# Optimization experiments

Measured on AMD Instinct MI355X. Metric: run time of the kernel, lower is better.

Reference implementation:

```python
import jax, jax.numpy as jnp
import numpy as np

N, E, H, IN_DIM, EDGE_DIM = 100000, 1600000, 64, 1, 1
SLOPE = 0.01  # leaky_relu negative slope (torch default; GATConv negative_slope=0.01)


def _lrelu(v):
    return jax.nn.leaky_relu(v, SLOPE)


def _segment_softmax(a, idx, num_segments):
    a_max = jax.ops.segment_max(a, idx, num_segments=num_segments)
    e = jnp.exp(a - a_max[idx])
    denom = jax.ops.segment_sum(e, idx, num_segments=num_segments)
    return e / denom[idx]


def _gru_cell(x, h, w_ih, w_hh, b_ih, b_hh):
    # torch.nn.GRUCell: gates ordered r, z, n
    gi = x @ w_ih.T + b_ih
    gh = h @ w_hh.T + b_hh
    i_r, i_z, i_n = jnp.split(gi, 3, axis=-1)
    h_r, h_z, h_n = jnp.split(gh, 3, axis=-1)
    r = jax.nn.sigmoid(i_r + h_r)
    z = jax.nn.sigmoid(i_z + h_z)
    n = jnp.tanh(i_n + r * h_n)
    return (1.0 - z) * n + z * h


def setup_inputs():
    key = jax.random.key(0)
    ks = jax.random.split(key, 20)
    s = 0.1
    p = lambda i, shape: s * jax.random.normal(ks[i], shape, jnp.float32)
    z = lambda shape: jnp.zeros(shape, jnp.float32)
    return {
        "node_attr": jax.random.normal(ks[0], (N, IN_DIM), jnp.float32),
        "edge_attr": jax.random.normal(ks[1], (E, EDGE_DIM), jnp.float32),
        "edge_index": jax.random.randint(ks[2], (2, E), 0, N, jnp.int32),
        "w1": p(3, (H, IN_DIM)), "b1": z((H,)),
        "wg1": p(4, (H, H + EDGE_DIM)), "att_l": p(5, (H,)), "att_r": p(6, (H,)),
        "wg2": p(7, (H, H)), "bg": z((H,)),
        "gru1_wih": p(8, (3 * H, H)), "gru1_whh": p(9, (3 * H, H)),
        "gru1_bih": z((3 * H,)), "gru1_bhh": z((3 * H,)),
        "wm": p(10, (H, H)), "att_src": p(11, (H,)), "att_dst": p(12, (H,)),
        "bm": z((H,)),
        "gru2_wih": p(13, (3 * H, H)), "gru2_whh": p(14, (3 * H, H)),
        "gru2_bih": z((3 * H,)), "gru2_bhh": z((3 * H,)),
        "w2": p(15, (H, H)), "b2": z((H,)),
    }


def _forward(node_attr, edge_attr, edge_index, w1, b1, wg1, att_l, att_r, wg2, bg,
             gru1_wih, gru1_whh, gru1_bih, gru1_bhh,
             wm, att_src, att_dst, bm,
             gru2_wih, gru2_whh, gru2_bih, gru2_bhh, w2, b2):
    src, dst = edge_index[0], edge_index[1]
    # lin1 + in-place leaky_relu
    x = _lrelu(node_attr @ w1.T + b1)                                      # [N,H]
    # --- GATEConv: gather -> edge transform -> softmax over dst -> scatter-add ---
    h_e = _lrelu(jnp.concatenate([x[src], edge_attr], axis=-1) @ wg1.T)    # [E,H]
    a = _lrelu(h_e @ att_l + x[dst] @ att_r)                               # [E]
    alpha = _segment_softmax(a, dst, N)
    h = jax.ops.segment_sum((h_e @ wg2.T) * alpha[:, None], dst, num_segments=N) + bg
    x = jax.nn.relu(_gru_cell(jax.nn.elu(h), x, gru1_wih, gru1_whh, gru1_bih, gru1_bhh))
    # --- molecule readout: batch = zeros(N) -> single graph ---
    batch = jnp.zeros((x.shape[0],), jnp.int32)
    out = jax.nn.relu(jax.ops.segment_sum(x, batch, num_segments=1))       # [1,H]
    # GATConv over bipartite graph (every node -> its graph), shared lin, 1 head
    xs = x @ wm.T                                                          # [N,H]
    xd = out @ wm.T                                                        # [1,H]
    a2 = _lrelu(xs @ att_src + (xd @ att_dst)[batch])                      # [N]
    alpha2 = _segment_softmax(a2, batch, 1)
    h2 = jax.ops.segment_sum(xs * alpha2[:, None], batch, num_segments=1) + bm
    out = jax.nn.relu(_gru_cell(jax.nn.elu(h2), out, gru2_wih, gru2_whh, gru2_bih, gru2_bhh))
    return out @ w2.T + b2                                                 # [1,H]


def reference(node_attr, edge_attr, edge_index, w1, b1, wg1, att_l, att_r, wg2, bg,
              gru1_wih, gru1_whh, gru1_bih, gru1_bhh,
              wm, att_src, att_dst, bm,
              gru2_wih, gru2_whh, gru2_bih, gru2_bhh, w2, b2):
    return _forward(node_attr, edge_attr, edge_index, w1, b1, wg1, att_l, att_r, wg2, bg,
                    gru1_wih, gru1_whh, gru1_bih, gru1_bhh,
                    wm, att_src, att_dst, bm,
                    gru2_wih, gru2_whh, gru2_bih, gru2_bhh, w2, b2)
```

## Files before the change

kernel.cpp:

```cpp
#include <hip/hip_runtime.h>
#include <math.h>

typedef __attribute__((ext_vector_type(8))) short bf8;
typedef __attribute__((ext_vector_type(4))) float f32x4;

#define BSHIFT 8

__device__ __forceinline__ float lrelu(float v){ return fmaxf(v, 0.01f * v); }

__device__ __forceinline__ float wave_sum(float v){
#pragma unroll
  for (int s = 32; s > 0; s >>= 1) v += __shfl_xor(v, s);
  return v;
}
__device__ __forceinline__ float wave_max(float v){
#pragma unroll
  for (int s = 32; s > 0; s >>= 1) v = fmaxf(v, __shfl_xor(v, s));
  return v;
}

__device__ __forceinline__ float bcast(float v, int k){
  return __uint_as_float((unsigned)__builtin_amdgcn_readlane(__float_as_uint(v), k));
}

__device__ __forceinline__ unsigned fkey(float x){
  unsigned u = __float_as_uint(x);
  return (u & 0x80000000u) ? ~u : (u | 0x80000000u);
}
__device__ __forceinline__ float funkey(unsigned k){
  unsigned u = (k & 0x80000000u) ? (k & 0x7fffffffu) : ~k;
  return __uint_as_float(u);
}

__device__ __forceinline__ short f2bfs(float x){
  unsigned u = __float_as_uint(x);
  return (short)((u + 0x7fffu + ((u >> 16) & 1u)) >> 16);
}
__device__ __forceinline__ float bf2f(ushort v){
  return __uint_as_float((unsigned)v << 16);
}
__device__ __forceinline__ bf8 pack8(float4 a, float4 b){
  bf8 v;
  v[0]=f2bfs(a.x); v[1]=f2bfs(a.y); v[2]=f2bfs(a.z); v[3]=f2bfs(a.w);
  v[4]=f2bfs(b.x); v[5]=f2bfs(b.y); v[6]=f2bfs(b.z); v[7]=f2bfs(b.w);
  return v;
}
__device__ __forceinline__ float4 xo4(float nav, float4 w, float4 b){
  float4 r;
  r.x = lrelu(nav*w.x + b.x); r.y = lrelu(nav*w.y + b.y);
  r.z = lrelu(nav*w.z + b.z); r.w = lrelu(nav*w.w + b.w);
  return r;
}
__device__ __forceinline__ float dot4(float4 a, float4 b){
  return a.x*b.x + a.y*b.y + a.z*b.z + a.w*b.w;
}

__global__ void k_wprep(const float* __restrict__ wg1, const float* __restrict__ wm,
                        const float* __restrict__ w2,
                        const float* __restrict__ g2wih, const float* __restrict__ g2whh,
                        float* __restrict__ wm_t, float* __restrict__ w2_t,
                        float* __restrict__ g2ih_t, float* __restrict__ g2hh_t,
                        float* __restrict__ wgc){
  int k = blockIdx.x;
  int r = threadIdx.x;
  if (r < 64){
    wm_t [k * 64 + r] = wm [r * 64 + k];
    w2_t [k * 64 + r] = w2 [r * 64 + k];
    if (k == 0) wgc[r] = wg1[r * 65 + 64];
  }
  g2ih_t[k * 192 + r] = g2wih[r * 64 + k];
  g2hh_t[k * 192 + r] = g2whh[r * 64 + k];
}

__global__ void k_wfrag(const float* __restrict__ wg2, const float* __restrict__ wm,
                        const float* __restrict__ wg1,
                        const float* __restrict__ wih, const float* __restrict__ whh,
                        ushort* __restrict__ wg2f, ushort* __restrict__ wmf,
                        ushort* __restrict__ wg1f,
                        ushort* __restrict__ wihf, ushort* __restrict__ whhf){
  int tid = blockIdx.x * 256 + threadIdx.x;
  if (tid >= 4608) return;
  const float* W; ushort* F; int T, S, base;
  if (tid < 512)      { W = wg2; F = wg2f; T = 4;  S = 64; base = tid; }
  else if (tid < 1024){ W = wm;  F = wmf;  T = 4;  S = 64; base = tid - 1024 + 512; }
  else if (tid < 1536){ W = wg1; F = wg1f; T = 4;  S = 65; base = tid - 1024; }
  else if (tid < 3072){ W = wih; F = wihf; T = 12; S = 64; base = tid - 1536; }
  else                { W = whh; F = whhf; T = 12; S = 64; base = tid - 3072; }
  int l  = base & 63;
  int ct = base >> 6;
  int c  = ct / T, t = ct - c * T;
  int row = 16 * t + (l & 15);
  int k0  = 32 * c + (l >> 4) * 8;
  const float* src = W + row * S + k0;
  unsigned o0 = (unsigned)(ushort)f2bfs(src[0]) | ((unsigned)(ushort)f2bfs(src[1]) << 16);
  unsigned o1 = (unsigned)(ushort)f2bfs(src[2]) | ((unsigned)(ushort)f2bfs(src[3]) << 16);
  unsigned o2 = (unsigned)(ushort)f2bfs(src[4]) | ((unsigned)(ushort)f2bfs(src[5]) << 16);
  unsigned o3 = (unsigned)(ushort)f2bfs(src[6]) | ((unsigned)(ushort)f2bfs(src[7]) << 16);
  ((uint4*)F)[base] = make_uint4(o0, o1, o2, o3);
}

__global__ __launch_bounds__(256) void k_node_m(
    const float* __restrict__ na, const float* __restrict__ w1,
    const float* __restrict__ b1, const ushort* __restrict__ wg1f,
    const float* __restrict__ att_r,
    ushort* __restrict__ yb, float* __restrict__ xr, int N){
  int lane = threadIdx.x & 63;
  int wid  = threadIdx.x >> 6;
  int m = lane & 15, g = lane >> 4;
  const bf8* WG = (const bf8*)wg1f;
  float4 w1a = *(const float4*)(w1 + g*8),      w1b = *(const float4*)(w1 + g*8 + 4);
  float4 w1c = *(const float4*)(w1 + 32 + g*8), w1d = *(const float4*)(w1 + 32 + g*8 + 4);
  float4 b1a = *(const float4*)(b1 + g*8),      b1b = *(const float4*)(b1 + g*8 + 4);
  float4 b1c = *(const float4*)(b1 + 32 + g*8), b1d = *(const float4*)(b1 + 32 + g*8 + 4);
  float4 ara = *(const float4*)(att_r + g*8),      arb = *(const float4*)(att_r + g*8 + 4);
  float4 arc = *(const float4*)(att_r + 32 + g*8), ard = *(const float4*)(att_r + 32 + g*8 + 4);
  int ntiles = (N + 15) >> 4;
  for (int tile = blockIdx.x * 4 + wid; tile < ntiles; tile += gridDim.x * 4){
    int n0 = tile * 16;
    int row = n0 + m;
    bool valid = row < N;
    float nav = valid ? na[row] : 0.f;
    float4 x0 = xo4(nav, w1a, b1a), x1 = xo4(nav, w1b, b1b);
    float4 x2 = xo4(nav, w1c, b1c), x3 = xo4(nav, w1d, b1d);
    float xa = dot4(x0, ara) + dot4(x1, arb) + dot4(x2, arc) + dot4(x3, ard);
    xa += __shfl_xor(xa, 16); xa += __shfl_xor(xa, 32);
    if (g == 0 && valid) xr[row] = xa;
    bf8 fa0 = pack8(x0, x1), fa1 = pack8(x2, x3);
    f32x4 yt[4];
#pragma unroll
    for (int t = 0; t < 4; t++){
      f32x4 acc = {0.f, 0.f, 0.f, 0.f};
      acc = __builtin_amdgcn_mfma_f32_16x16x32_bf16(fa0, WG[t * 64 + lane], acc, 0, 0, 0);
      acc = __builtin_amdgcn_mfma_f32_16x16x32_bf16(fa1, WG[(4 + t) * 64 + lane], acc, 0, 0, 0);
      yt[t] = acc;
    }
#pragma unroll
    for (int t = 0; t < 4; t++){
#pragma unroll
      for (int r = 0; r < 4; r++){
        int rw = n0 + g * 4 + r;
        if (rw < N) yb[(size_t)rw * 64 + m + 16 * t] = (ushort)f2bfs(yt[t][r]);
      }
    }
  }
}

__global__ __launch_bounds__(256) void k_bhist(const int* __restrict__ dst,
                                               int* __restrict__ bcnt, int E, int nbuck){
  __shared__ int hist[512];
  hist[threadIdx.x] = 0; hist[256 + threadIdx.x] = 0;
  __syncthreads();
  int e0 = blockIdx.x * 4096;
  int e1 = min(e0 + 4096, E);
  for (int i = e0 + threadIdx.x; i < e1; i += 256)
    atomicAdd(&hist[dst[i] >> BSHIFT], 1);
  __syncthreads();
#pragma unroll
  for (int q = 0; q < 2; q++){
    int j = threadIdx.x + q * 256;
    if (j < nbuck && hist[j] > 0) atomicAdd(&bcnt[j], hist[j]);
  }
}

__global__ void k_bscan(const int* __restrict__ bcnt, int* __restrict__ bbase,
                        int* __restrict__ gtail, int nbuck){
  __shared__ int lds[512];
  int t = threadIdx.x;
  int v = (t < nbuck) ? bcnt[t] : 0;
  lds[t] = v;
  __syncthreads();
  for (int s = 1; s < 512; s <<= 1){
    int tv = (t >= s) ? lds[t - s] : 0;
    __syncthreads();
    lds[t] += tv;
    __syncthreads();
  }
  if (t <= nbuck){
    int excl = (t == 0) ? 0 : lds[t - 1];
    bbase[t] = excl;
    if (t < nbuck) gtail[t] = excl;
  }
}

__global__ __launch_bounds__(256) void k_binA(
    const int* __restrict__ dst, const int* __restrict__ src,
    const float* __restrict__ ea, int* __restrict__ gtail,
    int2* __restrict__ tse, int E){
  __shared__ int hist[512], base[512], run[512];
  int e0 = blockIdx.x * 4096;
  int e1 = min(e0 + 4096, E);
  hist[threadIdx.x] = 0; hist[256 + threadIdx.x] = 0;
  run[threadIdx.x] = 0;  run[256 + threadIdx.x] = 0;
  __syncthreads();
  for (int i = e0 + threadIdx.x; i < e1; i += 256)
    atomicAdd(&hist[dst[i] >> BSHIFT], 1);
  __syncthreads();
#pragma unroll
  for (int q = 0; q < 2; q++){
    int j = threadIdx.x + q * 256;
    if (hist[j] > 0) base[j] = atomicAdd(&gtail[j], hist[j]);
  }
  __syncthreads();
  for (int i = e0 + threadIdx.x; i < e1; i += 256){
    int d = dst[i];
    int b = d >> BSHIFT;
    int pos = base[b] + atomicAdd(&run[b], 1);
    tse[pos] = make_int2(src[i] | ((d & 255) << 17), __float_as_int(ea[i]));
  }
}

__global__ __launch_bounds__(256) void k_binB(
    const int* __restrict__ bbase, const int2* __restrict__ tse,
    int2* __restrict__ csr, int* __restrict__ off, int N){
  __shared__ int degL[256];
  __shared__ int fillL[256];
  int node0 = blockIdx.x << BSHIFT;
  int node1 = min(node0 + 256, N);
  int nn = node1 - node0;
  int i0 = bbase[blockIdx.x], i1 = bbase[blockIdx.x + 1];
  int t = threadIdx.x;
  degL[t] = 0;
  __syncthreads();
  for (int i = i0 + t; i < i1; i += 256)
    atomicAdd(&degL[(tse[i].x >> 17) & 255], 1);
  __syncthreads();
  for (int s = 1; s < 256; s <<= 1){
    int v = (t >= s) ? degL[t - s] : 0;
    __syncthreads();
    degL[t] += v;
    __syncthreads();
  }
  int prev = (t == 0) ? 0 : degL[t - 1];
  fillL[t] = i0 + prev;
  if (t < nn) off[node0 + t] = i0 + prev;
  if (t == 0 && node1 == N) off[N] = i1;
  __syncthreads();
  for (int i = i0 + t; i < i1; i += 256){
    int2 rec = tse[i];
    int drel = (rec.x >> 17) & 255;
    int pos = atomicAdd(&fillL[drel], 1);
    csr[pos] = make_int2(rec.x & 0x1FFFF, rec.y);
  }
}

__global__ void k_edge_f(const int* __restrict__ off, const int2* __restrict__ csr,
                         const ushort* __restrict__ yb, const float* __restrict__ xr,
                         const float* __restrict__ wgc, const float* __restrict__ att_l,
                         float* __restrict__ sout, int N){
  int lane = threadIdx.x & 63;
  int wwid = (blockIdx.x * blockDim.x + threadIdx.x) >> 6;
  int g = lane >> 4, sl = lane & 15;
  int node = wwid * 4 + g;
  if (node >= N) return;
  int i0 = off[node], i1 = off[node + 1];
  float4 wc4 = ((const float4*)wgc)[sl];
  float4 al4 = ((const float4*)att_l)[sl];
  float xrn = xr[node];
  float sg = 0.f;
  float4 acc = make_float4(0.f, 0.f, 0.f, 0.f);
  int cnt = i1 - i0;
  int2 rA = make_int2(0,0), rB = rA, rC = rA, rD = rA;
  ushort4 yA = make_ushort4(0,0,0,0), yB = yA, yC = yA, yD = yA;
  if (cnt > 0){ rA = csr[i0];     yA = ((const ushort4*)(yb + (size_t)rA.x * 64))[sl]; }
  if (cnt > 1){ rB = csr[i0 + 1]; yB = ((const ushort4*)(yb + (size_t)rB.x * 64))[sl]; }
  if (cnt > 2){ rC = csr[i0 + 2]; yC = ((const ushort4*)(yb + (size_t)rC.x * 64))[sl]; }
  if (cnt > 3){ rD = csr[i0 + 3]; yD = ((const ushort4*)(yb + (size_t)rD.x * 64))[sl]; }
  int i = i0;
  for (; i + 1 < i1; i += 2){
    float eaA = __int_as_float(rA.y);
    float eaB = __int_as_float(rB.y);
    float4 heA, heB;
    heA.x = lrelu(bf2f(yA.x) + eaA * wc4.x); heB.x = lrelu(bf2f(yB.x) + eaB * wc4.x);
    heA.y = lrelu(bf2f(yA.y) + eaA * wc4.y); heB.y = lrelu(bf2f(yB.y) + eaB * wc4.y);
    heA.z = lrelu(bf2f(yA.z) + eaA * wc4.z); heB.z = lrelu(bf2f(yB.z) + eaB * wc4.z);
    heA.w = lrelu(bf2f(yA.w) + eaA * wc4.w); heB.w = lrelu(bf2f(yB.w) + eaB * wc4.w);
    rA = rC; yA = yC; rB = rD; yB = yD;
    if (i + 4 < i1){ rC = csr[i + 4]; yC = ((const ushort4*)(yb + (size_t)rC.x * 64))[sl]; }
    if (i + 5 < i1){ rD = csr[i + 5]; yD = ((const ushort4*)(yb + (size_t)rD.x * 64))[sl]; }
    float pA = dot4(heA, al4), pB = dot4(heB, al4);
    pA += __shfl_xor(pA, 1); pB += __shfl_xor(pB, 1);
    pA += __shfl_xor(pA, 2); pB += __shfl_xor(pB, 2);
    pA += __shfl_xor(pA, 4); pB += __shfl_xor(pB, 4);
    pA += __shfl_xor(pA, 8); pB += __shfl_xor(pB, 8);
    float wa = __expf(lrelu(pA + xrn));
    float wb = __expf(lrelu(pB + xrn));
    sg += wa + wb;
    acc.x += wa * heA.x + wb * heB.x;
    acc.y += wa * heA.y + wb * heB.y;
    acc.z += wa * heA.z + wb * heB.z;
    acc.w += wa * heA.w + wb * heB.w;
  }
  if (i < i1){
    float ea = __int_as_float(rA.y);
    float4 he;
    he.x = lrelu(bf2f(yA.x) + ea * wc4.x);
    he.y = lrelu(bf2f(yA.y) + ea * wc4.y);
    he.z = lrelu(bf2f(yA.z) + ea * wc4.z);
    he.w = lrelu(bf2f(yA.w) + ea * wc4.w);
    float p = dot4(he, al4);
    p += __shfl_xor(p, 1); p += __shfl_xor(p, 2);
    p += __shfl_xor(p, 4); p += __shfl_xor(p, 8);
    float w = __expf(lrelu(p + xrn));
    sg += w;
    acc.x += w * he.x; acc.y += w * he.y;
    acc.z += w * he.z; acc.w += w * he.w;
  }
  float inv = (i1 > i0 && sg > 0.f) ? 1.f / sg : 0.f;
  float4 o = make_float4(acc.x * inv, acc.y * inv, acc.z * inv, acc.w * inv);
  ((float4*)(sout + (size_t)node * 64))[sl] = o;
}

__global__ __launch_bounds__(256) void k_gru1m(
    const float* __restrict__ sout, const float* __restrict__ na,
    const float* __restrict__ w1, const float* __restrict__ b1,
    const ushort* __restrict__ wg2f, const float* __restrict__ bg,
    const ushort* __restrict__ wihf, const ushort* __restrict__ whhf,
    const float* __restrict__ bih, const float* __restrict__ bhh,
    float* __restrict__ x2, int N){
  __shared__ ushort xgl[4][16][72];
  int lane = threadIdx.x & 63;
  int wid  = threadIdx.x >> 6;
  int m = lane & 15, g = lane >> 4;
  int n0 = blockIdx.x * 64 + wid * 16;
  if (n0 >= N) return;
  int rowc = min(n0 + m, N - 1);
  const float* srow = sout + (size_t)rowc * 64;
  bf8 sa0 = pack8(*(const float4*)(srow + g * 8),      *(const float4*)(srow + g * 8 + 4));
  bf8 sa1 = pack8(*(const float4*)(srow + 32 + g * 8), *(const float4*)(srow + 32 + g * 8 + 4));
  const bf8* WG = (const bf8*)wg2f;
  f32x4 h[4];
#pragma unroll
  for (int t = 0; t < 4; t++){
    f32x4 acc = {0.f, 0.f, 0.f, 0.f};
    acc = __builtin_amdgcn_mfma_f32_16x16x32_bf16(sa0, WG[t * 64 + lane], acc, 0, 0, 0);
    acc = __builtin_amdgcn_mfma_f32_16x16x32_bf16(sa1, WG[(4 + t) * 64 + lane], acc, 0, 0, 0);
    h[t] = acc;
  }
#pragma unroll
  for (int t = 0; t < 4; t++){
    float bgc = bg[m + 16 * t];
#pragma unroll
    for (int r = 0; r < 4; r++){
      float hv = h[t][r] + bgc;
      float xg = hv > 0.f ? hv : __expf(hv) - 1.f;
      xgl[wid][g * 4 + r][m + 16 * t] = (ushort)f2bfs(xg);
    }
  }
  float nav = na[rowc];
  bf8 xoa0 = pack8(xo4(nav, *(const float4*)(w1 + g * 8),      *(const float4*)(b1 + g * 8)),
                   xo4(nav, *(const float4*)(w1 + g * 8 + 4),  *(const float4*)(b1 + g * 8 + 4)));
  bf8 xoa1 = pack8(xo4(nav, *(const float4*)(w1 + 32 + g * 8),     *(const float4*)(b1 + 32 + g * 8)),
                   xo4(nav, *(const float4*)(w1 + 32 + g * 8 + 4), *(const float4*)(b1 + 32 + g * 8 + 4)));
  bf8 xga0 = *(const bf8*)&xgl[wid][m][g * 8];
  bf8 xga1 = *(const bf8*)&xgl[wid][m][32 + g * 8];
  const bf8* WI = (const bf8*)wihf;
  const bf8* WH = (const bf8*)whhf;
#pragma unroll
  for (int t = 0; t < 4; t++){
    f32x4 iR = {0.f,0.f,0.f,0.f}, iZ = iR, iN = iR, hR = iR, hZ = iR, hN = iR;
    iR = __builtin_amdgcn_mfma_f32_16x16x32_bf16(xga0, WI[(t     ) * 64 + lane], iR, 0,0,0);
    iR = __builtin_amdgcn_mfma_f32_16x16x32_bf16(xga1, WI[(12 + t) * 64 + lane], iR, 0,0,0);
    iZ = __builtin_amdgcn_mfma_f32_16x16x32_bf16(xga0, WI[(t +  4) * 64 + lane], iZ, 0,0,0);
    iZ = __builtin_amdgcn_mfma_f32_16x16x32_bf16(xga1, WI[(16 + t) * 64 + lane], iZ, 0,0,0);
    iN = __builtin_amdgcn_mfma_f32_16x16x32_bf16(xga0, WI[(t +  8) * 64 + lane], iN, 0,0,0);
    iN = __builtin_amdgcn_mfma_f32_16x16x32_bf16(xga1, WI[(20 + t) * 64 + lane], iN, 0,0,0);
    hR = __builtin_amdgcn_mfma_f32_16x16x32_bf16(xoa0, WH[(t     ) * 64 + lane], hR, 0,0,0);
    hR = __builtin_amdgcn_mfma_f32_16x16x32_bf16(xoa1, WH[(12 + t) * 64 + lane], hR, 0,0,0);
    hZ = __builtin_amdgcn_mfma_f32_16x16x32_bf16(xoa0, WH[(t +  4) * 64 + lane], hZ, 0,0,0);
    hZ = __builtin_amdgcn_mfma_f32_16x16x32_bf16(xoa1, WH[(16 + t) * 64 + lane], hZ, 0,0,0);
    hN = __builtin_amdgcn_mfma_f32_16x16x32_bf16(xoa0, WH[(t +  8) * 64 + lane], hN, 0,0,0);
    hN = __builtin_amdgcn_mfma_f32_16x16x32_bf16(xoa1, WH[(20 + t) * 64 + lane], hN, 0,0,0);
    int col = m + 16 * t;
    float biR = bih[col], biZ = bih[64 + col], biN = bih[128 + col];
    float bhR = bhh[col], bhZ = bhh[64 + col], bhN = bhh[128 + col];
    float w1c = w1[col], b1c = b1[col];
#pragma unroll
    for (int r = 0; r < 4; r++){
      int node = n0 + g * 4 + r;
      if (node < N){
        float xon = lrelu(na[node] * w1c + b1c);
        float rg = 1.f / (1.f + __expf(-(iR[r] + biR + hR[r] + bhR)));
        float zg = 1.f / (1.f + __expf(-(iZ[r] + biZ + hZ[r] + bhZ)));
        float nn = tanhf(iN[r] + biN + rg * (hN[r] + bhN));
        float xn = (1.f - zg) * nn + zg * xon;
        x2[(size_t)node * 64 + col] = fmaxf(xn, 0.f);
      }
    }
  }
}

__global__ __launch_bounds__(256) void k_part2m(
    float* __restrict__ xb,
    const ushort* __restrict__ wmf, const float* __restrict__ att_src,
    float* __restrict__ tb, float* __restrict__ scal, int N){
  int lane = threadIdx.x & 63;
  int wid  = threadIdx.x >> 6;
  int m = lane & 15, g = lane >> 4;
  const bf8* WM = (const bf8*)wmf;
  float as_t[4];
#pragma unroll
  for (int t = 0; t < 4; t++) as_t[t] = att_src[m + 16 * t];
  float os[16];
#pragma unroll
  for (int j = 0; j < 16; j++) os[j] = 0.f;
  float tmax = -1e30f;
  int ntiles = (N + 15) >> 4;
  for (int tile = blockIdx.x * 4 + wid; tile < ntiles; tile += gridDim.x * 4){
    int n0 = tile * 16;
    int row = n0 + m;
    bool valid = row < N;
    int rowc = valid ? row : (N - 1);
    const float* xrow = xb + (size_t)rowc * 64;
    float4 a0 = *(const float4*)(xrow + g * 8);
    float4 a1 = *(const float4*)(xrow + g * 8 + 4);
    float4 a2 = *(const float4*)(xrow + 32 + g * 8);
    float4 a3 = *(const float4*)(xrow + 32 + g * 8 + 4);
    if (!valid){ a0 = make_float4(0,0,0,0); a1 = a0; a2 = a0; a3 = a0; }
    os[0]+=a0.x; os[1]+=a0.y; os[2]+=a0.z; os[3]+=a0.w;
    os[4]+=a1.x; os[5]+=a1.y; os[6]+=a1.z; os[7]+=a1.w;
    os[8]+=a2.x; os[9]+=a2.y; os[10]+=a2.z; os[11]+=a2.w;
    os[12]+=a3.x; os[13]+=a3.y; os[14]+=a3.z; os[15]+=a3.w;
    bf8 fa0 = pack8(a0, a1), fa1 = pack8(a2, a3);
    f32x4 xs_t[4];
#pragma unroll
    for (int t = 0; t < 4; t++){
      f32x4 acc = {0.f, 0.f, 0.f, 0.f};
      acc = __builtin_amdgcn_mfma_f32_16x16x32_bf16(fa0, WM[t * 64 + lane], acc, 0, 0, 0);
      acc = __builtin_amdgcn_mfma_f32_16x16x32_bf16(fa1, WM[(4 + t) * 64 + lane], acc, 0, 0, 0);
      xs_t[t] = acc;
    }
    float tpart[4] = {0.f, 0.f, 0.f, 0.f};
#pragma unroll
    for (int t = 0; t < 4; t++){
#pragma unroll
      for (int r = 0; r < 4; r++){
        int rw = n0 + g * 4 + r;
        if (rw < N) xb[(size_t)rw * 64 + m + 16 * t] = xs_t[t][r];
        tpart[r] += xs_t[t][r] * as_t[t];
      }
    }
#pragma unroll
    for (int r = 0; r < 4; r++){
      float v = tpart[r];
      v += __shfl_xor(v, 1); v += __shfl_xor(v, 2);
      v += __shfl_xor(v, 4); v += __shfl_xor(v, 8);
      if (m == 0){
        int rw = n0 + g * 4 + r;
        if (rw < N){ tb[rw] = v; tmax = fmaxf(tmax, v); }
      }
    }
  }
  tmax = wave_max(tmax);
  if (lane == 0) atomicMax((unsigned*)(scal + 131), fkey(tmax));
#pragma unroll
  for (int j = 0; j < 16; j++){
    float v = os[j];
    v += __shfl_xor(v, 1); v += __shfl_xor(v, 2);
    v += __shfl_xor(v, 4); v += __shfl_xor(v, 8);
    os[j] = v;
  }
  __shared__ float osm[4][64];
  if (m == 0){
#pragma unroll
    for (int j = 0; j < 8; j++){
      osm[wid][g * 8 + j]      = os[j];
      osm[wid][32 + g * 8 + j] = os[8 + j];
    }
  }
  __syncthreads();
  if (threadIdx.x < 64)
    atomicAdd(&scal[threadIdx.x],
              osm[0][threadIdx.x] + osm[1][threadIdx.x] + osm[2][threadIdx.x] + osm[3][threadIdx.x]);
}

__global__ void k_part2b(float* __restrict__ scal, const float* __restrict__ wm_t,
                         const float* __restrict__ att_dst){
  int lane = threadIdx.x;
  float o = fmaxf(scal[lane], 0.f);
  float acc = 0.f;
  for (int k = 0; k < 64; k++) acc += bcast(o, k) * wm_t[k * 64 + lane];
  float c = wave_sum(acc * att_dst[lane]);
  scal[64 + lane] = o;
  if (lane == 0){
    scal[128] = c;
    float maxtb = funkey(*(unsigned*)(scal + 131));
    scal[130] = lrelu(maxtb + c);
  }
}

__global__ void k_a2sum(const float* __restrict__ tb, const float* __restrict__ xs,
                        float* __restrict__ scal, int N){
  int lane = threadIdx.x & 63, w = threadIdx.x >> 6;
  int gw = blockIdx.x * 4 + w, nw = gridDim.x * 4;
  float c = scal[128];
  float M = scal[130];
  float hloc = 0.f, sloc = 0.f;
  for (int n = gw; n < N; n += nw){
    float a2 = lrelu(tb[n] + c);
    float wt = __expf(a2 - M);
    sloc += wt;
    hloc += wt * xs[(size_t)n * 64 + lane];
  }
  __shared__ float lds[256];
  __shared__ float sred[4];
  lds[threadIdx.x] = hloc;
  if (lane == 0) sred[w] = sloc;
  __syncthreads();
  if (threadIdx.x < 64)
    atomicAdd(&scal[192 + threadIdx.x],
              lds[threadIdx.x] + lds[64 + threadIdx.x] + lds[128 + threadIdx.x] + lds[192 + threadIdx.x]);
  if (threadIdx.x == 0) atomicAdd(&scal[129], sred[0] + sred[1] + sred[2] + sred[3]);
}

__global__ void k_final(const float* __restrict__ scal, const float* __restrict__ bm,
                        const float* __restrict__ g2ih_t, const float* __restrict__ g2hh_t,
                        const float* __restrict__ bih, const float* __restrict__ bhh,
                        const float* __restrict__ w2_t, const float* __restrict__ b2,
                        float* __restrict__ dout){
  int lane = threadIdx.x;
  float S  = scal[129];
  float h2 = scal[192 + lane] / S + bm[lane];
  float xg = h2 > 0.f ? h2 : __expf(h2) - 1.f;
  float xo = scal[64 + lane];
  float gir = bih[lane], giz = bih[64 + lane], gin = bih[128 + lane];
  float ghr = bhh[lane], ghz = bhh[64 + lane], ghn = bhh[128 + lane];
  for (int k = 0; k < 64; k++){
    float a = bcast(xg, k), b = bcast(xo, k);
    const float* gi = g2ih_t + k * 192;
    const float* gh = g2hh_t + k * 192;
    gir += a * gi[lane]; giz += a * gi[64 + lane]; gin += a * gi[128 + lane];
    ghr += b * gh[lane]; ghz += b * gh[64 + lane]; ghn += b * gh[128 + lane];
  }
  float r  = 1.f / (1.f + __expf(-(gir + ghr)));
  float z  = 1.f / (1.f + __expf(-(giz + ghz)));
  float nn = tanhf(gin + r * ghn);
  float o2 = fmaxf((1.f - z) * nn + z * xo, 0.f);
  float res = 0.f;
  for (int k = 0; k < 64; k++) res += bcast(o2, k) * w2_t[k * 64 + lane];
  dout[lane] = res + b2[lane];
}

extern "C" void kernel_launch(void* const* d_in, const int* in_sizes, int n_in,
                              void* d_out, int out_size, void* d_ws, size_t ws_size,
                              hipStream_t stream){
  const float* na    = (const float*)d_in[0];
  const float* ea    = (const float*)d_in[1];
  const int*   ei    = (const int*)d_in[2];
  const float* w1    = (const float*)d_in[3];
  const float* b1    = (const float*)d_in[4];
  const float* wg1   = (const float*)d_in[5];
  const float* att_l = (const float*)d_in[6];
  const float* att_r = (const float*)d_in[7];
  const float* wg2   = (const float*)d_in[8];
  const float* bg    = (const float*)d_in[9];
  const float* g1wih = (const float*)d_in[10];
  const float* g1whh = (const float*)d_in[11];
  const float* g1bih = (const float*)d_in[12];
  const float* g1bhh = (const float*)d_in[13];
  const float* wm      = (const float*)d_in[14];
  const float* att_src = (const float*)d_in[15];
  const float* att_dst = (const float*)d_in[16];
  const float* bm      = (const float*)d_in[17];
  const float* g2wih = (const float*)d_in[18];
  const float* g2whh = (const float*)d_in[19];
  const float* g2bih = (const float*)d_in[20];
  const float* g2bhh = (const float*)d_in[21];
  const float* w2    = (const float*)d_in[22];
  const float* b2    = (const float*)d_in[23];

  int N = in_sizes[0];
  int E = in_sizes[1];
  const int* srcArr = ei;
  const int* dstArr = ei + E;

  char* ws = (char*)d_ws;
  size_t cur = 0;
  auto alloc = [&](size_t nbytes) -> char* {
    char* p = ws + cur;
    cur += (nbytes + 255) & ~(size_t)255;
    return p;
  };
  ushort* yb   = (ushort*)alloc((size_t)N * 64 * 2);
  float* bufC  = (float*)alloc((size_t)N * 64 * 4);
  float* xr    = (float*)alloc((size_t)N * 4);
  float* tb    = (float*)alloc((size_t)N * 4);
  int*   offA  = (int*)alloc((size_t)(N + 1) * 4);
  int*   bcnt  = (int*)alloc(4096);
  int*   bbase = (int*)alloc(4096);
  int*   gtail = (int*)alloc(4096);
  int2*  csr   = (int2*)alloc((size_t)E * 8);
  int2*  tse   = (int2*)alloc((size_t)E * 8);
  float* scal  = (float*)alloc(4096);
  float* wm_t  = (float*)alloc(64 * 64 * 4);
  float* w2_t  = (float*)alloc(64 * 64 * 4);
  float* g2ih_t= (float*)alloc(64 * 192 * 4);
  float* g2hh_t= (float*)alloc(64 * 192 * 4);
  float* wgc   = (float*)alloc(64 * 4);
  ushort* wg2f = (ushort*)alloc(4096 * 2);
  ushort* wmf  = (ushort*)alloc(4096 * 2);
  ushort* wg1f = (ushort*)alloc(4096 * 2);
  ushort* wihf = (ushort*)alloc(12288 * 2);
  ushort* whhf = (ushort*)alloc(12288 * 2);
  if (cur > ws_size) return;

  hipMemsetAsync(bcnt, 0, 4096, stream);
  hipMemsetAsync(scal, 0, 4096, stream);

  k_wprep<<<64, 192, 0, stream>>>(wg1, wm, w2, g2wih, g2whh,
                                  wm_t, w2_t, g2ih_t, g2hh_t, wgc);
  k_wfrag<<<18, 256, 0, stream>>>(wg2, wm, wg1, g1wih, g1whh,
                                  wg2f, wmf, wg1f, wihf, whhf);

  int nbuck = (N + 255) >> BSHIFT;
  k_node_m<<<512, 256, 0, stream>>>(na, w1, b1, wg1f, att_r, yb, xr, N);
  k_bhist<<<(E + 4095) / 4096, 256, 0, stream>>>(dstArr, bcnt, E, nbuck);
  k_bscan<<<1, 512, 0, stream>>>(bcnt, bbase, gtail, nbuck);
  k_binA<<<(E + 4095) / 4096, 256, 0, stream>>>(dstArr, srcArr, ea, gtail, tse, E);
  k_binB<<<nbuck, 256, 0, stream>>>(bbase, tse, csr, offA, N);
  int nwb2 = (N + 15) / 16;
  k_edge_f<<<nwb2, 256, 0, stream>>>(offA, csr, yb, xr, wgc, att_l, bufC, N);
  int ngb = (N + 63) / 64;
  k_gru1m<<<ngb, 256, 0, stream>>>(bufC, na, w1, b1, wg2f, bg, wihf, whhf,
                                   g1bih, g1bhh, bufC, N);
  k_part2m<<<512, 256, 0, stream>>>(bufC, wmf, att_src, tb, scal, N);
  k_part2b<<<1, 64, 0, stream>>>(scal, wm_t, att_dst);
  k_a2sum<<<512, 256, 0, stream>>>(tb, bufC, scal, N);
  k_final<<<1, 64, 0, stream>>>(scal, bm, g2ih_t, g2hh_t, g2bih, g2bhh, w2_t, b2, (float*)d_out);
  (void)n_in; (void)out_size;
}
```

Baseline: 233.7 us.

## Sort nodes by degree for balanced edge aggregation and fuse histogram into node kernel

Adds a degree histogram in k_binB, a 64-bin scan and a counting-sort fill that builds a permutation of nodes grouped by in-degree. k_edge_f then processes nodes in that order, so the four 16-lane groups in a wavefront handle nodes of similar degree and less divergence from uneven loop lengths. Separately, the destination bucket histogram is merged into the node MFMA kernel as extra blocks, saving one launch. The cost is two extra small kernels, an indirection load per node, and less locality in the per-node writes.

```diff
diff --git a/kernel.cpp b/kernel.cpp
--- a/kernel.cpp
+++ b/kernel.cpp
@@ -99,11 +99,29 @@
   ((uint4*)F)[base] = make_uint4(o0, o1, o2, o3);
 }
 
-__global__ __launch_bounds__(256) void k_node_m(
+__global__ __launch_bounds__(256) void k_node_bh(
     const float* __restrict__ na, const float* __restrict__ w1,
     const float* __restrict__ b1, const ushort* __restrict__ wg1f,
     const float* __restrict__ att_r,
-    ushort* __restrict__ yb, float* __restrict__ xr, int N){
+    ushort* __restrict__ yb, float* __restrict__ xr, int N,
+    const int* __restrict__ dst, int* __restrict__ bcnt, int E, int nbuck){
+  if (blockIdx.x >= 512){
+    __shared__ int hist[512];
+    hist[threadIdx.x] = 0; hist[256 + threadIdx.x] = 0;
+    __syncthreads();
+    int bid = blockIdx.x - 512;
+    int e0 = bid * 4096;
+    int e1 = min(e0 + 4096, E);
+    for (int i = e0 + threadIdx.x; i < e1; i += 256)
+      atomicAdd(&hist[dst[i] >> BSHIFT], 1);
+    __syncthreads();
+#pragma unroll
+    for (int q = 0; q < 2; q++){
+      int j = threadIdx.x + q * 256;
+      if (j < nbuck && hist[j] > 0) atomicAdd(&bcnt[j], hist[j]);
+    }
+    return;
+  }
   int lane = threadIdx.x & 63;
   int wid  = threadIdx.x >> 6;
   int m = lane & 15, g = lane >> 4;
@@ -115,7 +133,7 @@
   float4 ara = *(const float4*)(att_r + g*8),      arb = *(const float4*)(att_r + g*8 + 4);
   float4 arc = *(const float4*)(att_r + 32 + g*8), ard = *(const float4*)(att_r + 32 + g*8 + 4);
   int ntiles = (N + 15) >> 4;
-  for (int tile = blockIdx.x * 4 + wid; tile < ntiles; tile += gridDim.x * 4){
+  for (int tile = blockIdx.x * 4 + wid; tile < ntiles; tile += 512 * 4){
     int n0 = tile * 16;
     int row = n0 + m;
     bool valid = row < N;
@@ -145,23 +163,6 @@
   }
 }
 
-__global__ __launch_bounds__(256) void k_bhist(const int* __restrict__ dst,
-                                               int* __restrict__ bcnt, int E, int nbuck){
-  __shared__ int hist[512];
-  hist[threadIdx.x] = 0; hist[256 + threadIdx.x] = 0;
-  __syncthreads();
-  int e0 = blockIdx.x * 4096;
-  int e1 = min(e0 + 4096, E);
-  for (int i = e0 + threadIdx.x; i < e1; i += 256)
-    atomicAdd(&hist[dst[i] >> BSHIFT], 1);
-  __syncthreads();
-#pragma unroll
-  for (int q = 0; q < 2; q++){
-    int j = threadIdx.x + q * 256;
-    if (j < nbuck && hist[j] > 0) atomicAdd(&bcnt[j], hist[j]);
-  }
-}
-
 __global__ void k_bscan(const int* __restrict__ bcnt, int* __restrict__ bbase,
                         int* __restrict__ gtail, int nbuck){
   __shared__ int lds[512];
@@ -211,19 +212,23 @@
 
 __global__ __launch_bounds__(256) void k_binB(
     const int* __restrict__ bbase, const int2* __restrict__ tse,
-    int2* __restrict__ csr, int* __restrict__ off, int N){
+    int2* __restrict__ csr, int* __restrict__ off, int* __restrict__ dcnt, int N){
   __shared__ int degL[256];
   __shared__ int fillL[256];
+  __shared__ int dh[64];
   int node0 = blockIdx.x << BSHIFT;
   int node1 = min(node0 + 256, N);
   int nn = node1 - node0;
   int i0 = bbase[blockIdx.x], i1 = bbase[blockIdx.x + 1];
   int t = threadIdx.x;
   degL[t] = 0;
+  if (t < 64) dh[t] = 0;
   __syncthreads();
   for (int i = i0 + t; i < i1; i += 256)
     atomicAdd(&degL[(tse[i].x >> 17) & 255], 1);
   __syncthreads();
+  int rawdeg = degL[t];
+  if (t < nn) atomicAdd(&dh[min(rawdeg, 63)], 1);
   for (int s = 1; s < 256; s <<= 1){
     int v = (t >= s) ? degL[t - s] : 0;
     __syncthreads();
@@ -235,6 +240,7 @@
   if (t < nn) off[node0 + t] = i0 + prev;
   if (t == 0 && node1 == N) off[N] = i1;
   __syncthreads();
+  if (t < 64 && dh[t] > 0) atomicAdd(&dcnt[t], dh[t]);
   for (int i = i0 + t; i < i1; i += 256){
     int2 rec = tse[i];
     int drel = (rec.x >> 17) & 255;
@@ -243,15 +249,52 @@
   }
 }
 
+__global__ void k_dscan(const int* __restrict__ dcnt, int* __restrict__ dtail){
+  __shared__ int lds[64];
+  int t = threadIdx.x;
+  lds[t] = dcnt[t];
+  __syncthreads();
+  for (int s = 1; s < 64; s <<= 1){
+    int v = (t >= s) ? lds[t - s] : 0;
+    __syncthreads();
+    lds[t] += v;
+    __syncthreads();
+  }
+  dtail[t] = (t == 0) ? 0 : lds[t - 1];
+}
+
+__global__ __launch_bounds__(256) void k_dfill(const int* __restrict__ off,
+                                               int* __restrict__ dtail,
+                                               int* __restrict__ perm, int N){
+  __shared__ int hist[64], base[64], run[64];
+  int n0 = blockIdx.x * 4096;
+  int n1 = min(n0 + 4096, N);
+  if (threadIdx.x < 64){ hist[threadIdx.x] = 0; run[threadIdx.x] = 0; }
+  __syncthreads();
+  for (int n = n0 + threadIdx.x; n < n1; n += 256)
+    atomicAdd(&hist[min(off[n + 1] - off[n], 63)], 1);
+  __syncthreads();
+  if (threadIdx.x < 64 && hist[threadIdx.x] > 0)
+    base[threadIdx.x] = atomicAdd(&dtail[threadIdx.x], hist[threadIdx.x]);
+  __syncthreads();
+  for (int n = n0 + threadIdx.x; n < n1; n += 256){
+    int c = min(off[n + 1] - off[n], 63);
+    int pos = base[c] + atomicAdd(&run[c], 1);
+    perm[pos] = n;
+  }
+}
+
 __global__ void k_edge_f(const int* __restrict__ off, const int2* __restrict__ csr,
                          const ushort* __restrict__ yb, const float* __restrict__ xr,
                          const float* __restrict__ wgc, const float* __restrict__ att_l,
+                         const int* __restrict__ perm,
                          float* __restrict__ sout, int N){
   int lane = threadIdx.x & 63;
   int wwid = (blockIdx.x * blockDim.x + threadIdx.x) >> 6;
   int g = lane >> 4, sl = lane & 15;
-  int node = wwid * 4 + g;
-  if (node >= N) return;
+  int idx = wwid * 4 + g;
+  if (idx >= N) return;
+  int node = perm[idx];
   int i0 = off[node], i1 = off[node + 1];
   float4 wc4 = ((const float4*)wgc)[sl];
   float4 al4 = ((const float4*)att_l)[sl];
@@ -585,9 +628,12 @@
   float* xr    = (float*)alloc((size_t)N * 4);
   float* tb    = (float*)alloc((size_t)N * 4);
   int*   offA  = (int*)alloc((size_t)(N + 1) * 4);
+  int*   perm  = (int*)alloc((size_t)N * 4);
   int*   bcnt  = (int*)alloc(4096);
   int*   bbase = (int*)alloc(4096);
   int*   gtail = (int*)alloc(4096);
+  int*   dcnt  = (int*)alloc(256);
+  int*   dtail = (int*)alloc(256);
   int2*  csr   = (int2*)alloc((size_t)E * 8);
   int2*  tse   = (int2*)alloc((size_t)E * 8);
   float* scal  = (float*)alloc(4096);
@@ -604,6 +650,7 @@
   if (cur > ws_size) return;
 
   hipMemsetAsync(bcnt, 0, 4096, stream);
+  hipMemsetAsync(dcnt, 0, 256, stream);
   hipMemsetAsync(scal, 0, 4096, stream);
 
   k_wprep<<<64, 192, 0, stream>>>(wg1, wm, w2, g2wih, g2whh,
@@ -612,13 +659,16 @@
                                   wg2f, wmf, wg1f, wihf, whhf);
 
   int nbuck = (N + 255) >> BSHIFT;
-  k_node_m<<<512, 256, 0, stream>>>(na, w1, b1, wg1f, att_r, yb, xr, N);
-  k_bhist<<<(E + 4095) / 4096, 256, 0, stream>>>(dstArr, bcnt, E, nbuck);
+  int nbA = (E + 4095) / 4096;
+  k_node_bh<<<512 + nbA, 256, 0, stream>>>(na, w1, b1, wg1f, att_r, yb, xr, N,
+                                           dstArr, bcnt, E, nbuck);
   k_bscan<<<1, 512, 0, stream>>>(bcnt, bbase, gtail, nbuck);
-  k_binA<<<(E + 4095) / 4096, 256, 0, stream>>>(dstArr, srcArr, ea, gtail, tse, E);
-  k_binB<<<nbuck, 256, 0, stream>>>(bbase, tse, csr, offA, N);
+  k_binA<<<nbA, 256, 0, stream>>>(dstArr, srcArr, ea, gtail, tse, E);
+  k_binB<<<nbuck, 256, 0, stream>>>(bbase, tse, csr, offA, dcnt, N);
+  k_dscan<<<1, 64, 0, stream>>>(dcnt, dtail);
+  k_dfill<<<(N + 4095) / 4096, 256, 0, stream>>>(offA, dtail, perm, N);
   int nwb2 = (N + 15) / 16;
-  k_edge_f<<<nwb2, 256, 0, stream>>>(offA, csr, yb, xr, wgc, att_l, bufC, N);
+  k_edge_f<<<nwb2, 256, 0, stream>>>(offA, csr, yb, xr, wgc, att_l, perm, bufC, N);
   int ngb = (N + 63) / 64;
   k_gru1m<<<ngb, 256, 0, stream>>>(bufC, na, w1, b1, wg2f, bg, wihf, whhf,
                                    g1bih, g1bhh, bufC, N);
```

Measured after the change: 237.6 us. About the same (+1.7%).
